# Kernel optimization log

Measured on AMD Instinct MI355X. Metric: run time of the kernel, lower is better.

The kernel has to match this reference:

```python
import jax, jax.numpy as jnp
import numpy as np

E, V, F, D = 500000, 50000, 100000, 128

def setup_inputs() -> dict:
    key = jax.random.key(0)
    ks = jax.random.split(key, 8)
    return {
        "prev_m_f_to_v": jax.random.normal(ks[0], (E, D), jnp.float32),
        "variable": jax.random.normal(ks[1], (V, D), jnp.float32),
        "factor": jax.random.normal(ks[2], (F, D), jnp.float32),
        "edge_attr": jax.random.normal(ks[3], (E, D), jnp.float32),
        "v_to_f": jax.random.randint(ks[4], (E,), 0, V, jnp.int32),
        "f_to_v": jax.random.randint(ks[5], (E,), 0, F, jnp.int32),
        "Wv": jax.random.normal(ks[6], (3 * D, D), jnp.float32) * (1.0 / np.sqrt(3 * D)),
        "bv": jnp.zeros((D,), jnp.float32),
        "Wf": jax.random.normal(ks[7], (3 * D, D), jnp.float32) * (1.0 / np.sqrt(3 * D)),
        "bf": jnp.zeros((D,), jnp.float32),
    }

def _mlp(x, y, edge_attr, W, b):
    # update(): concat along features then Linear(3d->d) + relu
    h = jnp.concatenate((x, y, edge_attr), axis=-1)  # [E, 3D]
    return jax.nn.relu(h @ W + b)                    # [E, D]

def reference(prev_m_f_to_v, variable, factor, edge_attr, v_to_f, f_to_v, Wv, bv, Wf, bf):
    nV = variable.shape[0]
    nF = factor.shape[0]
    # scatter-sum of factor->variable messages onto variables
    sum_f_to_v = jax.ops.segment_sum(prev_m_f_to_v, v_to_f, num_segments=nV)  # [V, D]
    # BP exclusion: gather back and subtract own message
    m_v_to_f = sum_f_to_v[v_to_f] - prev_m_f_to_v                             # [E, D]
    m_v_to_f = _mlp(variable[v_to_f], m_v_to_f, edge_attr, Wv, bv)            # [E, D]
    # scatter-sum of variable->factor messages onto factors
    sum_v_to_f = jax.ops.segment_sum(m_v_to_f, f_to_v, num_segments=nF)       # [F, D]
    m_f_to_v = sum_v_to_f[f_to_v] - m_v_to_f                                  # [E, D]
    m_f_to_v = _mlp(factor[f_to_v], m_f_to_v, edge_attr, Wf, bf)              # [E, D]
    new_factor = sum_v_to_f + factor
    new_variable = sum_f_to_v + variable
    return (m_f_to_v, new_factor, new_variable)
```

## Files before the change

### kernel.cpp

```cpp
#include <hip/hip_runtime.h>

typedef __attribute__((ext_vector_type(8))) __bf16 bf16x8;
typedef __attribute__((ext_vector_type(4))) __bf16 bf16x4;
typedef __attribute__((ext_vector_type(2))) __bf16 bf16x2;
typedef __attribute__((ext_vector_type(4))) float f32x4;

__device__ __forceinline__ void gload_lds16(const void* g, void* l) {
    __builtin_amdgcn_global_load_lds(
        (const __attribute__((address_space(1))) void*)g,
        (__attribute__((address_space(3))) void*)l, 16, 0, 0);
}

__device__ inline bf16x8 pack8(f32x4 u0, f32x4 u1) {
    bf16x8 r;
    r[0] = (__bf16)u0[0]; r[1] = (__bf16)u0[1]; r[2] = (__bf16)u0[2]; r[3] = (__bf16)u0[3];
    r[4] = (__bf16)u1[0]; r[5] = (__bf16)u1[1]; r[6] = (__bf16)u1[2]; r[7] = (__bf16)u1[3];
    return r;
}

__global__ void pack_w(const float* __restrict__ W, __bf16* __restrict__ out,
                       int baseA, float sA, int baseB, float sB) {
    int i = blockIdx.x * blockDim.x + threadIdx.x;
    if (i >= 256 * 128) return;
    int k = i >> 7, d = i & 127;
    float v = (k < 128) ? sA * W[(long)(baseA + k) * 128 + d]
                        : sB * W[(long)(baseB + (k - 128)) * 128 + d];
    int t = k >> 5, n = d >> 4;
    int lane = (d & 15) | (((k >> 3) & 3) << 4);
    int j = k & 7;
    out[((long)(t * 8 + n) * 64 + lane) * 8 + j] = (__bf16)v;
}


__global__ void hist_kernel(const int* __restrict__ v_to_f, const int* __restrict__ f_to_v,
                            int* __restrict__ counts, int V, int E) {
    int stride = gridDim.x * blockDim.x;
    for (int e = blockIdx.x * blockDim.x + threadIdx.x; e < E; e += stride) {
        atomicAdd(&counts[v_to_f[e]], 1);
        atomicAdd(&counts[V + f_to_v[e]], 1);
    }
}

#define SCAN_BLOCK 256
#define SCAN_ELEMS 4

__global__ void scan_pass1(const int* __restrict__ counts, int* __restrict__ partials, int N) {
    int t = threadIdx.x;
    int base = blockIdx.x * (SCAN_BLOCK * SCAN_ELEMS) + t * SCAN_ELEMS;
    int s = 0;
#pragma unroll
    for (int j = 0; j < SCAN_ELEMS; ++j) {
        int i = base + j;
        if (i < N) s += counts[i];
    }
#pragma unroll
    for (int off = 1; off < 64; off <<= 1) s += __shfl_xor(s, off);
    __shared__ int lds[4];
    if ((t & 63) == 0) lds[t >> 6] = s;
    __syncthreads();
    if (t == 0) partials[blockIdx.x] = lds[0] + lds[1] + lds[2] + lds[3];
}

__global__ void scan_pass2(int* __restrict__ partials, int nb, int* __restrict__ offsets,
                           int N, int total) {
    int t = threadIdx.x;
    int v = (t < nb) ? partials[t] : 0;
    int lane = t & 63, w = t >> 6;
    int x = v;
#pragma unroll
    for (int off = 1; off < 64; off <<= 1) { int y = __shfl_up(x, off); if (lane >= off) x += y; }
    __shared__ int lds[4];
    if (lane == 63) lds[w] = x;
    __syncthreads();
    int add = 0;
    for (int i = 0; i < w; ++i) add += lds[i];
    if (t < nb) partials[t] = x + add - v;
    if (t == 0) offsets[N] = total;
}

__global__ void scan_pass3(const int* __restrict__ counts, const int* __restrict__ partials,
                           int* __restrict__ offsets, int* __restrict__ cursors, int N) {
    int t = threadIdx.x;
    int base = blockIdx.x * (SCAN_BLOCK * SCAN_ELEMS) + t * SCAN_ELEMS;
    int c[SCAN_ELEMS];
    int s = 0;
#pragma unroll
    for (int j = 0; j < SCAN_ELEMS; ++j) {
        int i = base + j;
        c[j] = (i < N) ? counts[i] : 0;
        s += c[j];
    }
    int lane = t & 63, w = t >> 6;
    int x = s;
#pragma unroll
    for (int off = 1; off < 64; off <<= 1) { int y = __shfl_up(x, off); if (lane >= off) x += y; }
    __shared__ int lds[4];
    if (lane == 63) lds[w] = x;
    __syncthreads();
    int add = 0;
    for (int i = 0; i < w; ++i) add += lds[i];
    int run = x + add - s + partials[blockIdx.x];
#pragma unroll
    for (int j = 0; j < SCAN_ELEMS; ++j) {
        int i = base + j;
        if (i < N) { offsets[i] = run; cursors[i] = run; }
        run += c[j];
    }
}

__global__ void fill_kernel(const int* __restrict__ v_to_f, const int* __restrict__ f_to_v,
                            int* __restrict__ cursors, int* __restrict__ bucket, int V, int E) {
    int stride = gridDim.x * blockDim.x;
    for (int e = blockIdx.x * blockDim.x + threadIdx.x; e < E; e += stride) {
        int p = atomicAdd(&cursors[v_to_f[e]], 1);
        bucket[p] = e;
        int q = atomicAdd(&cursors[V + f_to_v[e]], 1);
        bucket[q] = e;
    }
}


__global__ __launch_bounds__(256) void gsum_f32(
    const float* __restrict__ src, const int* __restrict__ bucket,
    const int* __restrict__ offsets, int toff,
    const float* __restrict__ addtab, float* __restrict__ sumout,
    float* __restrict__ addout, int T) {
    int gw = (int)((blockIdx.x * (long)blockDim.x + threadIdx.x) >> 6);
    if (gw >= T) return;
    int lane = threadIdx.x & 63;
    int start = offsets[toff + gw], end = offsets[toff + gw + 1];
    float ax = 0.f, ay = 0.f, bx = 0.f, by = 0.f;
    int i = start;
    for (; i + 1 < end; i += 2) {
        int e0 = bucket[i], e1 = bucket[i + 1];
        float2 v0 = *(const float2*)(src + (long)e0 * 128 + lane * 2);
        float2 v1 = *(const float2*)(src + (long)e1 * 128 + lane * 2);
        ax += v0.x; ay += v0.y; bx += v1.x; by += v1.y;
    }
    if (i < end) {
        int e0 = bucket[i];
        float2 v0 = *(const float2*)(src + (long)e0 * 128 + lane * 2);
        ax += v0.x; ay += v0.y;
    }
    ax += bx; ay += by;
    long o = (long)gw * 128 + lane * 2;
    *(float2*)(sumout + o) = make_float2(ax, ay);
    float2 a = *(const float2*)(addtab + o);
    *(float2*)(addout + o) = make_float2(ax + a.x, ay + a.y);
}

__global__ __launch_bounds__(256) void gsum_bf16(
    const __bf16* __restrict__ src, const int* __restrict__ bucket,
    const int* __restrict__ offsets, int toff,
    const float* __restrict__ addtab, float* __restrict__ sumout,
    float* __restrict__ addout, int T) {
    int gw = (int)((blockIdx.x * (long)blockDim.x + threadIdx.x) >> 6);
    if (gw >= T) return;
    int lane = threadIdx.x & 63;
    int start = offsets[toff + gw], end = offsets[toff + gw + 1];
    float ax = 0.f, ay = 0.f, bx = 0.f, by = 0.f;
    int i = start;
    for (; i + 1 < end; i += 2) {
        int e0 = bucket[i], e1 = bucket[i + 1];
        bf16x2 v0 = *(const bf16x2*)(src + (long)e0 * 128 + lane * 2);
        bf16x2 v1 = *(const bf16x2*)(src + (long)e1 * 128 + lane * 2);
        ax += (float)v0[0]; ay += (float)v0[1];
        bx += (float)v1[0]; by += (float)v1[1];
    }
    if (i < end) {
        int e0 = bucket[i];
        bf16x2 v0 = *(const bf16x2*)(src + (long)e0 * 128 + lane * 2);
        ax += (float)v0[0]; ay += (float)v0[1];
    }
    ax += bx; ay += by;
    long o = (long)gw * 128 + lane * 2;
    *(float2*)(sumout + o) = make_float2(ax, ay);
    float2 a = *(const float2*)(addtab + o);
    *(float2*)(addout + o) = make_float2(ax + a.x, ay + a.y);
}

__global__ __launch_bounds__(256, 4) void table_gemm(
    const float* __restrict__ src0, const float* __restrict__ src1,
    const __bf16* __restrict__ WT, const float* __restrict__ bias,
    __bf16* __restrict__ out, int T) {
    const int wave = threadIdx.x >> 6;
    const int lane = threadIdx.x & 63;
    const int row = lane & 15;
    const int kch = lane >> 4;
    const long wbase = ((long)blockIdx.x * 4 + wave) * 32;

    const float* p0[2]; const float* p1[2];
#pragma unroll
    for (int rb = 0; rb < 2; ++rb) {
        long r = wbase + rb * 16 + row;
        long rl = (r < T) ? r : (T - 1);
        p0[rb] = src0 + rl * 128 + kch * 8;
        p1[rb] = src1 + rl * 128 + kch * 8;
    }

    f32x4 acc[8][2];
#pragma unroll
    for (int n = 0; n < 8; ++n) {
        acc[n][0] = (f32x4){0.f, 0.f, 0.f, 0.f};
        acc[n][1] = (f32x4){0.f, 0.f, 0.f, 0.f};
    }

#pragma unroll
    for (int t = 0; t < 8; ++t) {
        bf16x8 a[2];
#pragma unroll
        for (int rb = 0; rb < 2; ++rb) {
            const float* p = (t < 4) ? (p0[rb] + t * 32) : (p1[rb] + (t - 4) * 32);
            f32x4 u0 = *(const f32x4*)p;
            f32x4 u1 = *(const f32x4*)(p + 4);
            a[rb] = pack8(u0, u1);
        }
        const __bf16* bbase = WT + (long)t * 8 * 512 + lane * 8;
#pragma unroll
        for (int n = 0; n < 8; ++n) {
            bf16x8 b = *(const bf16x8*)(bbase + n * 512);
            acc[n][0] = __builtin_amdgcn_mfma_f32_16x16x32_bf16(a[0], b, acc[n][0], 0, 0, 0);
            acc[n][1] = __builtin_amdgcn_mfma_f32_16x16x32_bf16(a[1], b, acc[n][1], 0, 0, 0);
        }
    }

    const int colbase = lane & 15;
    const int orow = (lane >> 4) * 4;
#pragma unroll
    for (int n = 0; n < 8; ++n) {
        int col = n * 16 + colbase;
        float bz = bias[col];
#pragma unroll
        for (int rb = 0; rb < 2; ++rb)
#pragma unroll
            for (int rr = 0; rr < 4; ++rr) {
                long r = wbase + rb * 16 + orow + rr;
                if (r < T) out[r * 128 + col] = (__bf16)(acc[n][rb][rr] + bz);
            }
    }
}

template <int PHASE>
__global__ __launch_bounds__(256, 4) void edge_gemm(
    const float* __restrict__ prevf, const __bf16* __restrict__ prevb,
    const float* __restrict__ eattr, const __bf16* __restrict__ WT,
    const __bf16* __restrict__ G, const int* __restrict__ idx,
    __bf16* __restrict__ outb, float* __restrict__ outf, int E) {
    __shared__ char lds[2][16384];
    const int wave = threadIdx.x >> 6;
    const int lane = threadIdx.x & 63;
    const int l16 = lane & 15;
    const int kch = lane >> 4;
    const long brow = (long)blockIdx.x * 128;

    auto stage = [&](int buf, int t) {
        char* dst = &lds[buf][0];
        if (PHASE == 2 && t < 4) {
#pragma unroll
            for (int q = 0; q < 2; ++q) {
                int s0 = q * 256 + wave * 64;
                int row = (s0 >> 2) + (lane >> 2);
                int c = lane & 3;
                int c2 = c ^ ((row >> 1) & 3);
                long rowg = brow + row; if (rowg >= E) rowg = E - 1;
                gload_lds16(prevb + rowg * 128 + t * 32 + c2 * 8, dst + s0 * 16);
            }
        } else {
            const float* srcb = (PHASE == 1 && t < 4) ? (prevf + t * 32)
                                                      : (eattr + (t - 4) * 32);
#pragma unroll
            for (int q = 0; q < 4; ++q) {
                int s0 = q * 256 + wave * 64;
                int row = (s0 >> 3) + (lane >> 3);
                int c = lane & 7;
                int c2 = c ^ (row & 7);
                long rowg = brow + row; if (rowg >= E) rowg = E - 1;
                gload_lds16(srcb + rowg * 128 + c2 * 4, dst + s0 * 16);
            }
        }
    };

    f32x4 acc[8][2];
#pragma unroll
    for (int n = 0; n < 8; ++n) {
        acc[n][0] = (f32x4){0.f, 0.f, 0.f, 0.f};
        acc[n][1] = (f32x4){0.f, 0.f, 0.f, 0.f};
    }

    stage(0, 0);
#pragma unroll
    for (int t = 0; t < 8; ++t) {
        __syncthreads();
        if (t < 7) stage((t + 1) & 1, t + 1);
        const char* cur = &lds[t & 1][0];
        bf16x8 a[2];
#pragma unroll
        for (int rb = 0; rb < 2; ++rb) {
            int row = wave * 32 + rb * 16 + l16;
            if (PHASE == 2 && t < 4) {
                int off = row * 64 + ((kch ^ ((row >> 1) & 3)) * 16);
                a[rb] = *(const bf16x8*)(cur + off);
            } else {
                int base = row * 128;
                int s0 = (((kch * 2 + 0) ^ (row & 7)) * 16);
                int s1 = (((kch * 2 + 1) ^ (row & 7)) * 16);
                f32x4 u0 = *(const f32x4*)(cur + base + s0);
                f32x4 u1 = *(const f32x4*)(cur + base + s1);
                a[rb] = pack8(u0, u1);
            }
        }
        const __bf16* bbase = WT + (long)t * 8 * 512 + lane * 8;
#pragma unroll
        for (int n = 0; n < 8; ++n) {
            bf16x8 b = *(const bf16x8*)(bbase + n * 512);
            acc[n][0] = __builtin_amdgcn_mfma_f32_16x16x32_bf16(a[0], b, acc[n][0], 0, 0, 0);
            acc[n][1] = __builtin_amdgcn_mfma_f32_16x16x32_bf16(a[1], b, acc[n][1], 0, 0, 0);
        }
    }

    __syncthreads();
    float* lbuf = (float*)((char*)lds + wave * 8192);
    const int slotcol = lane & 31;
    const int rhalf = lane >> 5;
#pragma unroll
    for (int rb = 0; rb < 2; ++rb) {
#pragma unroll
        for (int n = 0; n < 8; ++n)
#pragma unroll
            for (int rr = 0; rr < 4; ++rr) {
                int row = kch * 4 + rr;
                int col = n * 16 + l16;
                int slot = col >> 2;
                lbuf[row * 128 + (((slot ^ (row & 7)) << 2) | (col & 3))] = acc[n][rb][rr];
            }
#pragma unroll
        for (int j = 0; j < 8; ++j) {
            int row = 2 * j + rhalf;
            long eo = brow + wave * 32 + rb * 16 + row;
            f32x4 v = *(const f32x4*)&lbuf[row * 128 + ((slotcol ^ (row & 7)) << 2)];
            if (eo < E) {
                int g = idx[eo];
                bf16x4 gb = *(const bf16x4*)(G + (long)g * 128 + slotcol * 4);
                f32x4 o;
#pragma unroll
                for (int i = 0; i < 4; ++i) {
                    float x = v[i] + (float)gb[i];
                    o[i] = x > 0.f ? x : 0.f;
                }
                if (PHASE == 1) {
                    bf16x4 ob;
#pragma unroll
                    for (int i = 0; i < 4; ++i) ob[i] = (__bf16)o[i];
                    *(bf16x4*)(outb + eo * 128 + slotcol * 4) = ob;
                } else {
                    *(f32x4*)(outf + eo * 128 + slotcol * 4) = o;
                }
            }
        }
    }
}

extern "C" void kernel_launch(void* const* d_in, const int* in_sizes, int n_in,
                              void* d_out, int out_size, void* d_ws, size_t ws_size,
                              hipStream_t stream) {
    const float* prev_m   = (const float*)d_in[0];
    const float* variable = (const float*)d_in[1];
    const float* factor   = (const float*)d_in[2];
    const float* eattr    = (const float*)d_in[3];
    const int*   v_to_f   = (const int*)d_in[4];
    const int*   f_to_v   = (const int*)d_in[5];
    const float* Wv       = (const float*)d_in[6];
    const float* bv       = (const float*)d_in[7];
    const float* Wf       = (const float*)d_in[8];
    const float* bf       = (const float*)d_in[9];

    const int E = in_sizes[0] / 128;
    const int V = in_sizes[1] / 128;
    const int F = in_sizes[2] / 128;
    const int NT = V + F;

    float* out_m        = (float*)d_out;
    float* out_factor   = out_m + (long)E * 128;
    float* out_variable = out_factor + (long)F * 128;

    char* ws = (char*)d_ws;
    float* sum_f_to_v = (float*)ws;  ws += (long)V * 128 * 4;
    float* sum_v_to_f = (float*)ws;  ws += (long)F * 128 * 4;
    __bf16* m1        = (__bf16*)ws; ws += (long)E * 128 * 2;
    __bf16* G1        = (__bf16*)ws; ws += (long)V * 128 * 2;
    __bf16* G2        = (__bf16*)ws; ws += (long)F * 128 * 2;
    __bf16* Wtab_v    = (__bf16*)ws; ws += 256 * 128 * 2;
    __bf16* Wedge_v   = (__bf16*)ws; ws += 256 * 128 * 2;
    __bf16* Wtab_f    = (__bf16*)ws; ws += 256 * 128 * 2;
    __bf16* Wedge_f   = (__bf16*)ws; ws += 256 * 128 * 2;
    int* counts       = (int*)ws;    ws += (long)NT * 4;
    int* offsets      = (int*)ws;    ws += (long)(NT + 1) * 4;
    int* cursors      = (int*)ws;    ws += (long)NT * 4;
    int* bucket       = (int*)ws;    ws += (long)2 * E * 4;
    int* partials     = (int*)ws;    ws += 256 * 4;

    hipMemsetAsync(counts, 0, (size_t)NT * 4, stream);

    pack_w<<<dim3(128), dim3(256), 0, stream>>>(Wv, Wtab_v,  0,   1.f, 128, 1.f);
    pack_w<<<dim3(128), dim3(256), 0, stream>>>(Wv, Wedge_v, 128, -1.f, 256, 1.f);
    pack_w<<<dim3(128), dim3(256), 0, stream>>>(Wf, Wtab_f,  0,   1.f, 128, 1.f);
    pack_w<<<dim3(128), dim3(256), 0, stream>>>(Wf, Wedge_f, 128, -1.f, 256, 1.f);

    hist_kernel<<<dim3(2048), dim3(256), 0, stream>>>(v_to_f, f_to_v, counts, V, E);
    int nb = (NT + SCAN_BLOCK * SCAN_ELEMS - 1) / (SCAN_BLOCK * SCAN_ELEMS);
    scan_pass1<<<dim3(nb), dim3(SCAN_BLOCK), 0, stream>>>(counts, partials, NT);
    scan_pass2<<<dim3(1), dim3(SCAN_BLOCK), 0, stream>>>(partials, nb, offsets, NT, 2 * E);
    scan_pass3<<<dim3(nb), dim3(SCAN_BLOCK), 0, stream>>>(counts, partials, offsets, cursors, NT);
    fill_kernel<<<dim3(2048), dim3(256), 0, stream>>>(v_to_f, f_to_v, cursors, bucket, V, E);

    gsum_f32<<<dim3((V + 3) / 4), dim3(256), 0, stream>>>(
        prev_m, bucket, offsets, 0, variable, sum_f_to_v, out_variable, V);

    table_gemm<<<dim3((V + 127) / 128), dim3(256), 0, stream>>>(
        variable, sum_f_to_v, Wtab_v, bv, G1, V);

    int eblocks = (E + 127) / 128;
    edge_gemm<1><<<dim3(eblocks), dim3(256), 0, stream>>>(
        prev_m, nullptr, eattr, Wedge_v, G1, v_to_f, m1, nullptr, E);

    gsum_bf16<<<dim3((F + 3) / 4), dim3(256), 0, stream>>>(
        m1, bucket, offsets, V, factor, sum_v_to_f, out_factor, F);

    table_gemm<<<dim3((F + 127) / 128), dim3(256), 0, stream>>>(
        factor, sum_v_to_f, Wtab_f, bf, G2, F);

    edge_gemm<2><<<dim3(eblocks), dim3(256), 0, stream>>>(
        nullptr, m1, eattr, Wedge_f, G2, f_to_v, nullptr, out_m, E);
}
```

Measured before the change: 718.0 us.

## Pipeline edge GEMM per wave with triple-buffered LDS and register-prefetched weights

The edge GEMM drops block-wide __syncthreads double buffering. Each wave now stages its own 32 rows into a private triple-buffered LDS region, with explicit vmcnt waits and weight fragments prefetched into registers one step ahead. This targets barrier stalls and exposed load latency, at the cost of more registers and LDS, so occupancy drops to 3 blocks. The change also merges the four weight-pack launches into one, folds the middle scan pass into the last, and unrolls the gather-sum loops to four edges.

```diff
diff --git a/kernel.cpp b/kernel.cpp
--- a/kernel.cpp
+++ b/kernel.cpp
@@ -4,6 +4,8 @@
 typedef __attribute__((ext_vector_type(4))) __bf16 bf16x4;
 typedef __attribute__((ext_vector_type(2))) __bf16 bf16x2;
 typedef __attribute__((ext_vector_type(4))) float f32x4;
+
+template <int N> struct ic { static constexpr int value = N; };
 
 __device__ __forceinline__ void gload_lds16(const void* g, void* l) {
     __builtin_amdgcn_global_load_lds(
@@ -18,13 +20,20 @@
     return r;
 }
 
-__global__ void pack_w(const float* __restrict__ W, __bf16* __restrict__ out,
-                       int baseA, float sA, int baseB, float sB) {
-    int i = blockIdx.x * blockDim.x + threadIdx.x;
-    if (i >= 256 * 128) return;
+__global__ void pack_all(const float* __restrict__ Wv, const float* __restrict__ Wf,
+                         __bf16* __restrict__ Wtab_v, __bf16* __restrict__ Wedge_v,
+                         __bf16* __restrict__ Wtab_f, __bf16* __restrict__ Wedge_f) {
+    int which = blockIdx.x >> 7;
+    int i = ((blockIdx.x & 127) << 8) + threadIdx.x;
+    const float* W = (which < 2) ? Wv : Wf;
+    __bf16* out = (which == 0) ? Wtab_v : (which == 1) ? Wedge_v
+                 : (which == 2) ? Wtab_f : Wedge_f;
+    int baseA = (which & 1) ? 128 : 0;
+    float sA  = (which & 1) ? -1.f : 1.f;
+    int baseB = (which & 1) ? 256 : 128;
     int k = i >> 7, d = i & 127;
     float v = (k < 128) ? sA * W[(long)(baseA + k) * 128 + d]
-                        : sB * W[(long)(baseB + (k - 128)) * 128 + d];
+                        : W[(long)(baseB + (k - 128)) * 128 + d];
     int t = k >> 5, n = d >> 4;
     int lane = (d & 15) | (((k >> 3) & 3) << 4);
     int j = k & 7;
@@ -61,12 +70,23 @@
     if (t == 0) partials[blockIdx.x] = lds[0] + lds[1] + lds[2] + lds[3];
 }
 
-__global__ void scan_pass2(int* __restrict__ partials, int nb, int* __restrict__ offsets,
+__global__ void scan_pass3(const int* __restrict__ counts, const int* __restrict__ partials,
+                           int* __restrict__ offsets, int* __restrict__ cursors,
                            int N, int total) {
     int t = threadIdx.x;
-    int v = (t < nb) ? partials[t] : 0;
+    int pre = 0;
+    for (int i = 0; i < (int)blockIdx.x; ++i) pre += partials[i];
+    int base = blockIdx.x * (SCAN_BLOCK * SCAN_ELEMS) + t * SCAN_ELEMS;
+    int c[SCAN_ELEMS];
+    int s = 0;
+#pragma unroll
+    for (int j = 0; j < SCAN_ELEMS; ++j) {
+        int i = base + j;
+        c[j] = (i < N) ? counts[i] : 0;
+        s += c[j];
+    }
     int lane = t & 63, w = t >> 6;
-    int x = v;
+    int x = s;
 #pragma unroll
     for (int off = 1; off < 64; off <<= 1) { int y = __shfl_up(x, off); if (lane >= off) x += y; }
     __shared__ int lds[4];
@@ -74,38 +94,14 @@
     __syncthreads();
     int add = 0;
     for (int i = 0; i < w; ++i) add += lds[i];
-    if (t < nb) partials[t] = x + add - v;
-    if (t == 0) offsets[N] = total;
-}
-
-__global__ void scan_pass3(const int* __restrict__ counts, const int* __restrict__ partials,
-                           int* __restrict__ offsets, int* __restrict__ cursors, int N) {
-    int t = threadIdx.x;
-    int base = blockIdx.x * (SCAN_BLOCK * SCAN_ELEMS) + t * SCAN_ELEMS;
-    int c[SCAN_ELEMS];
-    int s = 0;
-#pragma unroll
-    for (int j = 0; j < SCAN_ELEMS; ++j) {
-        int i = base + j;
-        c[j] = (i < N) ? counts[i] : 0;
-        s += c[j];
-    }
-    int lane = t & 63, w = t >> 6;
-    int x = s;
-#pragma unroll
-    for (int off = 1; off < 64; off <<= 1) { int y = __shfl_up(x, off); if (lane >= off) x += y; }
-    __shared__ int lds[4];
-    if (lane == 63) lds[w] = x;
-    __syncthreads();
-    int add = 0;
-    for (int i = 0; i < w; ++i) add += lds[i];
-    int run = x + add - s + partials[blockIdx.x];
+    int run = x + add - s + pre;
 #pragma unroll
     for (int j = 0; j < SCAN_ELEMS; ++j) {
         int i = base + j;
         if (i < N) { offsets[i] = run; cursors[i] = run; }
         run += c[j];
     }
+    if (blockIdx.x == 0 && t == 0) offsets[N] = total;
 }
 
 __global__ void fill_kernel(const int* __restrict__ v_to_f, const int* __restrict__ f_to_v,
@@ -130,19 +126,23 @@
     int lane = threadIdx.x & 63;
     int start = offsets[toff + gw], end = offsets[toff + gw + 1];
     float ax = 0.f, ay = 0.f, bx = 0.f, by = 0.f;
+    float cx = 0.f, cy = 0.f, dx = 0.f, dy = 0.f;
     int i = start;
-    for (; i + 1 < end; i += 2) {
-        int e0 = bucket[i], e1 = bucket[i + 1];
+    for (; i + 3 < end; i += 4) {
+        int e0 = bucket[i], e1 = bucket[i + 1], e2 = bucket[i + 2], e3 = bucket[i + 3];
         float2 v0 = *(const float2*)(src + (long)e0 * 128 + lane * 2);
         float2 v1 = *(const float2*)(src + (long)e1 * 128 + lane * 2);
+        float2 v2 = *(const float2*)(src + (long)e2 * 128 + lane * 2);
+        float2 v3 = *(const float2*)(src + (long)e3 * 128 + lane * 2);
         ax += v0.x; ay += v0.y; bx += v1.x; by += v1.y;
-    }
-    if (i < end) {
+        cx += v2.x; cy += v2.y; dx += v3.x; dy += v3.y;
+    }
+    for (; i < end; ++i) {
         int e0 = bucket[i];
         float2 v0 = *(const float2*)(src + (long)e0 * 128 + lane * 2);
         ax += v0.x; ay += v0.y;
     }
-    ax += bx; ay += by;
+    ax += bx + cx + dx; ay += by + cy + dy;
     long o = (long)gw * 128 + lane * 2;
     *(float2*)(sumout + o) = make_float2(ax, ay);
     float2 a = *(const float2*)(addtab + o);
@@ -159,20 +159,23 @@
     int lane = threadIdx.x & 63;
     int start = offsets[toff + gw], end = offsets[toff + gw + 1];
     float ax = 0.f, ay = 0.f, bx = 0.f, by = 0.f;
+    float cx = 0.f, cy = 0.f, dx = 0.f, dy = 0.f;
     int i = start;
-    for (; i + 1 < end; i += 2) {
-        int e0 = bucket[i], e1 = bucket[i + 1];
+    for (; i + 3 < end; i += 4) {
+        int e0 = bucket[i], e1 = bucket[i + 1], e2 = bucket[i + 2], e3 = bucket[i + 3];
         bf16x2 v0 = *(const bf16x2*)(src + (long)e0 * 128 + lane * 2);
         bf16x2 v1 = *(const bf16x2*)(src + (long)e1 * 128 + lane * 2);
-        ax += (float)v0[0]; ay += (float)v0[1];
-        bx += (float)v1[0]; by += (float)v1[1];
-    }
-    if (i < end) {
+        bf16x2 v2 = *(const bf16x2*)(src + (long)e2 * 128 + lane * 2);
+        bf16x2 v3 = *(const bf16x2*)(src + (long)e3 * 128 + lane * 2);
+        ax += (float)v0[0]; ay += (float)v0[1]; bx += (float)v1[0]; by += (float)v1[1];
+        cx += (float)v2[0]; cy += (float)v2[1]; dx += (float)v3[0]; dy += (float)v3[1];
+    }
+    for (; i < end; ++i) {
         int e0 = bucket[i];
         bf16x2 v0 = *(const bf16x2*)(src + (long)e0 * 128 + lane * 2);
         ax += (float)v0[0]; ay += (float)v0[1];
     }
-    ax += bx; ay += by;
+    ax += bx + cx + dx; ay += by + cy + dy;
     long o = (long)gw * 128 + lane * 2;
     *(float2*)(sumout + o) = make_float2(ax, ay);
     float2 a = *(const float2*)(addtab + o);
@@ -241,45 +244,21 @@
 }
 
 template <int PHASE>
-__global__ __launch_bounds__(256, 4) void edge_gemm(
+__global__ __launch_bounds__(256, 3) void edge_gemm(
     const float* __restrict__ prevf, const __bf16* __restrict__ prevb,
     const float* __restrict__ eattr, const __bf16* __restrict__ WT,
     const __bf16* __restrict__ G, const int* __restrict__ idx,
     __bf16* __restrict__ outb, float* __restrict__ outf, int E) {
-    __shared__ char lds[2][16384];
+    __shared__ char lds[4][12288];
     const int wave = threadIdx.x >> 6;
     const int lane = threadIdx.x & 63;
     const int l16 = lane & 15;
     const int kch = lane >> 4;
     const long brow = (long)blockIdx.x * 128;
-
-    auto stage = [&](int buf, int t) {
-        char* dst = &lds[buf][0];
-        if (PHASE == 2 && t < 4) {
-#pragma unroll
-            for (int q = 0; q < 2; ++q) {
-                int s0 = q * 256 + wave * 64;
-                int row = (s0 >> 2) + (lane >> 2);
-                int c = lane & 3;
-                int c2 = c ^ ((row >> 1) & 3);
-                long rowg = brow + row; if (rowg >= E) rowg = E - 1;
-                gload_lds16(prevb + rowg * 128 + t * 32 + c2 * 8, dst + s0 * 16);
-            }
-        } else {
-            const float* srcb = (PHASE == 1 && t < 4) ? (prevf + t * 32)
-                                                      : (eattr + (t - 4) * 32);
-#pragma unroll
-            for (int q = 0; q < 4; ++q) {
-                int s0 = q * 256 + wave * 64;
-                int row = (s0 >> 3) + (lane >> 3);
-                int c = lane & 7;
-                int c2 = c ^ (row & 7);
-                long rowg = brow + row; if (rowg >= E) rowg = E - 1;
-                gload_lds16(srcb + rowg * 128 + c2 * 4, dst + s0 * 16);
-            }
-        }
-    };
-
+    const long wrow = brow + wave * 32;
+    char* wls = &lds[wave][0];
+
+    bf16x8 bufA[8], bufB[8];
     f32x4 acc[8][2];
 #pragma unroll
     for (int n = 0; n < 8; ++n) {
@@ -287,39 +266,77 @@
         acc[n][1] = (f32x4){0.f, 0.f, 0.f, 0.f};
     }
 
-    stage(0, 0);
-#pragma unroll
-    for (int t = 0; t < 8; ++t) {
-        __syncthreads();
-        if (t < 7) stage((t + 1) & 1, t + 1);
-        const char* cur = &lds[t & 1][0];
+    auto stage = [&](auto tcS) {
+        constexpr int S = decltype(tcS)::value;
+        char* dst = wls + (S % 3) * 4096;
+        if constexpr (PHASE == 2 && S < 4) {
+#pragma unroll
+            for (int q = 0; q < 2; ++q) {
+                int row = q * 16 + (lane >> 2);
+                int c2 = (lane & 3) ^ ((row >> 1) & 3);
+                long rg = wrow + row; if (rg >= E) rg = E - 1;
+                gload_lds16(prevb + rg * 128 + S * 32 + c2 * 8, dst + q * 1024);
+            }
+        } else {
+            const float* srcb = (PHASE == 1 && S < 4) ? (prevf + S * 32)
+                                                      : (eattr + (S - 4) * 32);
+#pragma unroll
+            for (int q = 0; q < 4; ++q) {
+                int row = q * 8 + (lane >> 3);
+                int c2 = (lane & 7) ^ (row & 7);
+                long rg = wrow + row; if (rg >= E) rg = E - 1;
+                gload_lds16(srcb + rg * 128 + c2 * 4, dst + q * 1024);
+            }
+        }
+    };
+
+    auto loadB = [&](auto tcT, bf16x8* bn) {
+        constexpr int T = decltype(tcT)::value;
+        const __bf16* bb = WT + (long)T * 4096 + lane * 8;
+#pragma unroll
+        for (int n = 0; n < 8; ++n) bn[n] = *(const bf16x8*)(bb + n * 512);
+    };
+
+    stage(ic<0>{});
+    __builtin_amdgcn_sched_barrier(0);
+    loadB(ic<0>{}, bufA);
+    __builtin_amdgcn_sched_barrier(0);
+    stage(ic<1>{});
+    __builtin_amdgcn_sched_barrier(0);
+
+    auto iter = [&](auto tcT) {
+        constexpr int T = decltype(tcT)::value;
+        constexpr int NS = (T < 7) ? (8 + ((PHASE == 2 && (T + 1) < 4) ? 2 : 4)) : 8;
+        asm volatile("s_waitcnt vmcnt(%0)" :: "n"(NS) : "memory");
+        __builtin_amdgcn_sched_barrier(0);
+        if constexpr (T < 7) loadB(ic<T + 1>{}, (T & 1) ? bufA : bufB);
+        __builtin_amdgcn_sched_barrier(0);
+        if constexpr (T < 6) stage(ic<T + 2>{});
+        __builtin_amdgcn_sched_barrier(0);
+        const char* cur = wls + (T % 3) * 4096;
         bf16x8 a[2];
 #pragma unroll
         for (int rb = 0; rb < 2; ++rb) {
-            int row = wave * 32 + rb * 16 + l16;
-            if (PHASE == 2 && t < 4) {
-                int off = row * 64 + ((kch ^ ((row >> 1) & 3)) * 16);
-                a[rb] = *(const bf16x8*)(cur + off);
+            int row = rb * 16 + l16;
+            if constexpr (PHASE == 2 && T < 4) {
+                a[rb] = *(const bf16x8*)(cur + row * 64 + ((kch ^ ((row >> 1) & 3)) * 16));
             } else {
-                int base = row * 128;
-                int s0 = (((kch * 2 + 0) ^ (row & 7)) * 16);
-                int s1 = (((kch * 2 + 1) ^ (row & 7)) * 16);
-                f32x4 u0 = *(const f32x4*)(cur + base + s0);
-                f32x4 u1 = *(const f32x4*)(cur + base + s1);
+                f32x4 u0 = *(const f32x4*)(cur + row * 128 + (((kch * 2) ^ (row & 7)) * 16));
+                f32x4 u1 = *(const f32x4*)(cur + row * 128 + (((kch * 2 + 1) ^ (row & 7)) * 16));
                 a[rb] = pack8(u0, u1);
             }
         }
-        const __bf16* bbase = WT + (long)t * 8 * 512 + lane * 8;
+        bf16x8* bc = (T & 1) ? bufB : bufA;
 #pragma unroll
         for (int n = 0; n < 8; ++n) {
-            bf16x8 b = *(const bf16x8*)(bbase + n * 512);
-            acc[n][0] = __builtin_amdgcn_mfma_f32_16x16x32_bf16(a[0], b, acc[n][0], 0, 0, 0);
-            acc[n][1] = __builtin_amdgcn_mfma_f32_16x16x32_bf16(a[1], b, acc[n][1], 0, 0, 0);
-        }
-    }
-
-    __syncthreads();
-    float* lbuf = (float*)((char*)lds + wave * 8192);
+            acc[n][0] = __builtin_amdgcn_mfma_f32_16x16x32_bf16(a[0], bc[n], acc[n][0], 0, 0, 0);
+            acc[n][1] = __builtin_amdgcn_mfma_f32_16x16x32_bf16(a[1], bc[n], acc[n][1], 0, 0, 0);
+        }
+    };
+    iter(ic<0>{}); iter(ic<1>{}); iter(ic<2>{}); iter(ic<3>{});
+    iter(ic<4>{}); iter(ic<5>{}); iter(ic<6>{}); iter(ic<7>{});
+
+    float* lbuf = (float*)wls;
     const int slotcol = lane & 31;
     const int rhalf = lane >> 5;
 #pragma unroll
@@ -336,7 +353,7 @@
 #pragma unroll
         for (int j = 0; j < 8; ++j) {
             int row = 2 * j + rhalf;
-            long eo = brow + wave * 32 + rb * 16 + row;
+            long eo = wrow + rb * 16 + row;
             f32x4 v = *(const f32x4*)&lbuf[row * 128 + ((slotcol ^ (row & 7)) << 2)];
             if (eo < E) {
                 int g = idx[eo];
@@ -401,16 +418,13 @@
 
     hipMemsetAsync(counts, 0, (size_t)NT * 4, stream);
 
-    pack_w<<<dim3(128), dim3(256), 0, stream>>>(Wv, Wtab_v,  0,   1.f, 128, 1.f);
-    pack_w<<<dim3(128), dim3(256), 0, stream>>>(Wv, Wedge_v, 128, -1.f, 256, 1.f);
-    pack_w<<<dim3(128), dim3(256), 0, stream>>>(Wf, Wtab_f,  0,   1.f, 128, 1.f);
-    pack_w<<<dim3(128), dim3(256), 0, stream>>>(Wf, Wedge_f, 128, -1.f, 256, 1.f);
+    pack_all<<<dim3(512), dim3(256), 0, stream>>>(Wv, Wf, Wtab_v, Wedge_v, Wtab_f, Wedge_f);
 
     hist_kernel<<<dim3(2048), dim3(256), 0, stream>>>(v_to_f, f_to_v, counts, V, E);
     int nb = (NT + SCAN_BLOCK * SCAN_ELEMS - 1) / (SCAN_BLOCK * SCAN_ELEMS);
     scan_pass1<<<dim3(nb), dim3(SCAN_BLOCK), 0, stream>>>(counts, partials, NT);
-    scan_pass2<<<dim3(1), dim3(SCAN_BLOCK), 0, stream>>>(partials, nb, offsets, NT, 2 * E);
-    scan_pass3<<<dim3(nb), dim3(SCAN_BLOCK), 0, stream>>>(counts, partials, offsets, cursors, NT);
+    scan_pass3<<<dim3(nb), dim3(SCAN_BLOCK), 0, stream>>>(counts, partials, offsets, cursors,
+                                                          NT, 2 * E);
     fill_kernel<<<dim3(2048), dim3(256), 0, stream>>>(v_to_f, f_to_v, cursors, bucket, V, E);
 
     gsum_f32<<<dim3((V + 3) / 4), dim3(256), 0, stream>>>(
```

New measurement: 713.4 us. Within noise of the previous version (-0.6%).
